# Performance work log

Measured on AMD Instinct MI355X. Metric: run time of the kernel, lower is better.

The kernel has to match this reference:

```python
import jax, jax.numpy as jnp
import numpy as np

B, T, D_IN, D_OUT = 4, 2048, 1024, 1024


def setup_inputs() -> dict:
    key = jax.random.key(0)
    k1, k2, k3, k4 = jax.random.split(key, 4)
    x = jax.random.normal(k1, (B, T, D_IN), dtype=jnp.float32)
    W_q = jax.random.normal(k2, (D_OUT, D_IN), dtype=jnp.float32) * 0.02
    W_k = jax.random.normal(k3, (D_OUT, D_IN), dtype=jnp.float32) * 0.02
    W_v = jax.random.normal(k4, (D_OUT, D_IN), dtype=jnp.float32) * 0.02
    return {"x": x, "W_q": W_q, "W_k": W_k, "W_v": W_v}


def reference(x, W_q, W_k, W_v):
    b, t, d_in = x.shape
    d_out = W_q.shape[0]
    # Linear projections (torch Linear: y = x @ W.T), no bias
    q = jnp.einsum("btd,od->bto", x, W_q)
    k = jnp.einsum("btd,od->bto", x, W_k)
    v = jnp.einsum("btd,od->bto", x, W_v)
    # Raw scores [b, t, t]
    scores = jnp.einsum("bqd,bkd->bqk", q, k)
    # Faithful to the source: tril with diagonal=1 => position i sees j <= i+1
    mask = jnp.tril(jnp.ones((t, t), dtype=bool), k=1)
    scores = jnp.where(mask, scores, -jnp.inf)
    # Scale by sqrt(d_out) (full d_out, single head), stable softmax
    attn = jax.nn.softmax(scores / jnp.sqrt(jnp.asarray(d_out, x.dtype)), axis=-1)
    # dropout=0.0 -> identity
    return jnp.einsum("bqk,bkd->bqd", attn, v)
```

## Files before the change

### kernel.cpp

```cpp
#include <hip/hip_runtime.h>
#include <hip/hip_bf16.h>

typedef unsigned short u16;
typedef __attribute__((ext_vector_type(8))) short short8v;
typedef __attribute__((ext_vector_type(4))) float float4v;

__device__ inline u16 f2b(float f) {
  __hip_bfloat16 h = __float2bfloat16(f);
  union { __hip_bfloat16 h; u16 s; } u;
  u.h = h;
  return u.s;
}

__device__ inline float b2f(u16 s) {
  union { u16 s[2]; float f; } u;
  u.s[0] = 0; u.s[1] = s;
  return u.f;
}

__device__ inline void gload_lds16(const u16* g, u16* l) {
  __builtin_amdgcn_global_load_lds(
      (const __attribute__((address_space(1))) void*)g,
      (__attribute__((address_space(3))) void*)l, 16, 0, 0);
}

__global__ __launch_bounds__(256) void cvt_f32_bf16(const float* __restrict__ in,
                                                    u16* __restrict__ out, int n4) {
  for (int i = blockIdx.x * blockDim.x + threadIdx.x; i < n4;
       i += gridDim.x * blockDim.x) {
    float4 v = ((const float4*)in)[i];
    ushort4 o;
    o.x = f2b(v.x); o.y = f2b(v.y); o.z = f2b(v.z); o.w = f2b(v.w);
    ((ushort4*)out)[i] = o;
  }
}

template <int MODE, typename CT>
__global__ __launch_bounds__(512)
void gemm4(const u16* __restrict__ A, int lda, long sA,
           const u16* __restrict__ B, int ldb, long sB,
           CT* __restrict__ C, int ldc, long sC, int K) {
  constexpr int BM = 256, BN = 128, BK = 64;
  constexpr int TILE_U16 = (BM + BN) * BK;
  constexpr int TILE_BYTES = TILE_U16 * 2;
  __shared__ __align__(16) u16 lds[3 * TILE_U16];

  const int z = blockIdx.z;
  A += (long)z * sA;
  B += (long)z * sB;

  int bx = blockIdx.x;
  if (MODE == 2) bx = gridDim.x - 1 - bx;
  const int m0 = bx * BM;
  const int n0 = blockIdx.y * BN;
  if (MODE == 1 && n0 > m0 + BM) return;
  int Keff = K;
  if (MODE == 2) Keff = min(m0 + BM + 1, K);
  const int nk = (Keff + BK - 1) >> 6;

  const int tid  = threadIdx.x;
  const int lane = tid & 63;
  const int wid  = tid >> 6;
  const int wr   = wid >> 1;
  const int wc   = wid & 1;

  const u16* gA[4]; int oA[4];
#pragma unroll
  for (int j = 0; j < 4; ++j) {
    int c = tid + j * 512;
    int r = c >> 3;
    int kg = ((c & 7) ^ (r & 7)) * 8;
    gA[j] = A + (long)(m0 + r) * lda + kg;
    oA[j] = c * 8;
  }
  const u16* gB[2]; int oB[2];
#pragma unroll
  for (int j = 0; j < 2; ++j) {
    int c = tid + j * 512;
    int r = c >> 3;
    int kg = ((c & 7) ^ (r & 7)) * 8;
    gB[j] = B + (long)(n0 + r) * ldb + kg;
    oB[j] = BM * BK + c * 8;
  }

  auto stageA3 = [&](int t, int buf) {
    const int k0 = t * BK;
    u16* base = lds + buf * TILE_U16;
    gload_lds16(gA[0] + k0, base + oA[0]);
    gload_lds16(gA[1] + k0, base + oA[1]);
    gload_lds16(gA[2] + k0, base + oA[2]);
  };
  auto stageRest = [&](int t, int buf) {
    const int k0 = t * BK;
    u16* base = lds + buf * TILE_U16;
    gload_lds16(gA[3] + k0, base + oA[3]);
    gload_lds16(gB[0] + k0, base + oB[0]);
    gload_lds16(gB[1] + k0, base + oB[1]);
  };

  const int rowA = wr * 64 + (lane & 15);
  const int rowB = wc * 64 + (lane & 15);
  const int msk  = (lane & 7) << 4;
  const int kl   = (lane >> 4) * 16;
  const int offA[2] = { rowA * 128 + ((kl) ^ msk),
                        rowA * 128 + ((64 + kl) ^ msk) };
  const int offB[2] = { 2 * BM * BK + rowB * 128 + ((kl) ^ msk),
                        2 * BM * BK + rowB * 128 + ((64 + kl) ^ msk) };

  float4v acc[4][4];
#pragma unroll
  for (int i = 0; i < 4; ++i)
#pragma unroll
    for (int j = 0; j < 4; ++j)
      acc[i][j] = (float4v){0.f, 0.f, 0.f, 0.f};

  stageA3(0, 0); stageRest(0, 0);
  if (nk > 1) { stageA3(1, 1); stageRest(1, 1); }

  int cur = 0;
  for (int t = 0; t < nk; ++t) {
    if (t + 1 < nk) asm volatile("s_waitcnt vmcnt(6)" ::: "memory");
    else            asm volatile("s_waitcnt vmcnt(0)" ::: "memory");
    __builtin_amdgcn_s_barrier();
    __builtin_amdgcn_sched_barrier(0);

    const char* bb = (const char*)lds + cur * TILE_BYTES;
    const int  nxt2 = (cur >= 1) ? cur - 1 : 2;
    const bool st   = (t + 2 < nk);

#pragma unroll
    for (int ks = 0; ks < 2; ++ks) {
      short8v a[4], b[4];
#pragma unroll
      for (int mi = 0; mi < 4; ++mi)
        a[mi] = *(const short8v*)(bb + offA[ks] + mi * 2048);
#pragma unroll
      for (int ni = 0; ni < 4; ++ni)
        b[ni] = *(const short8v*)(bb + offB[ks] + ni * 2048);
      if (ks == 0) { if (st) stageA3(t + 2, nxt2); }
      else         { if (st) stageRest(t + 2, nxt2); }
      __builtin_amdgcn_s_barrier();
      asm volatile("s_waitcnt lgkmcnt(0)" ::: "memory");
      __builtin_amdgcn_sched_barrier(0);
      __builtin_amdgcn_s_setprio(1);
#pragma unroll
      for (int mi = 0; mi < 4; ++mi)
#pragma unroll
        for (int ni = 0; ni < 4; ++ni)
          acc[mi][ni] = __builtin_amdgcn_mfma_f32_16x16x32_bf16(
              a[mi], b[ni], acc[mi][ni], 0, 0, 0);
      __builtin_amdgcn_s_setprio(0);
    }
    cur = (cur < 2) ? cur + 1 : 0;
  }

  CT* c = C + (long)z * sC;
  const int r0base = m0 + wr * 64 + ((lane >> 4) << 2);
  const int cbase  = n0 + wc * 64 + (lane & 15);
#pragma unroll
  for (int mi = 0; mi < 4; ++mi) {
#pragma unroll
    for (int ni = 0; ni < 4; ++ni) {
      const int r0 = r0base + mi * 16;
      const int cc = cbase + ni * 16;
#pragma unroll
      for (int r = 0; r < 4; ++r) {
        float v = acc[mi][ni][r];
        if constexpr (__is_same(CT, float)) c[(long)(r0 + r) * ldc + cc] = v;
        else                                c[(long)(r0 + r) * ldc + cc] = f2b(v);
      }
    }
  }
}

__global__ __launch_bounds__(256)
void softmax_kernel(u16* __restrict__ SP, int T) {
  const int  i    = blockIdx.x & (T - 1);
  const long base = (long)blockIdx.x * T;
  const int  nvis = min(i + 2, T);
  const int  capJ = min(T, ((i >> 8) << 8) + 320);
  const float scale = 0.03125f;

  __shared__ float red[4];

  const int j0 = threadIdx.x * 8;
  float v[8];
  float m = -INFINITY;
  if (j0 < nvis) {
    short8v raw = *(const short8v*)&SP[base + j0];
#pragma unroll
    for (int e = 0; e < 8; ++e) {
      float f = (j0 + e < nvis) ? b2f((u16)raw[e]) * scale : -INFINITY;
      v[e] = f;
      m = fmaxf(m, f);
    }
  }
#pragma unroll
  for (int o = 32; o; o >>= 1) m = fmaxf(m, __shfl_xor(m, o));
  const int wid = threadIdx.x >> 6;
  if ((threadIdx.x & 63) == 0) red[wid] = m;
  __syncthreads();
  m = fmaxf(fmaxf(red[0], red[1]), fmaxf(red[2], red[3]));
  __syncthreads();

  float s = 0.f;
  if (j0 < nvis) {
#pragma unroll
    for (int e = 0; e < 8; ++e) {
      float p = (j0 + e < nvis) ? __expf(v[e] - m) : 0.f;
      v[e] = p;
      s += p;
    }
  }
#pragma unroll
  for (int o = 32; o; o >>= 1) s += __shfl_xor(s, o);
  if ((threadIdx.x & 63) == 0) red[wid] = s;
  __syncthreads();
  s = red[0] + red[1] + red[2] + red[3];
  const float inv = 1.0f / s;

  if (j0 < capJ) {
    short8v o8;
#pragma unroll
    for (int e = 0; e < 8; ++e)
      o8[e] = (short)f2b((j0 + e < nvis) ? v[e] * inv : 0.f);
    *(short8v*)&SP[base + j0] = o8;
  }
}

extern "C" void kernel_launch(void* const* d_in, const int* in_sizes, int n_in,
                              void* d_out, int out_size, void* d_ws, size_t ws_size,
                              hipStream_t stream) {
  const float* x  = (const float*)d_in[0];
  const float* Wq = (const float*)d_in[1];
  const float* Wk = (const float*)d_in[2];
  const float* Wv = (const float*)d_in[3];
  float* out = (float*)d_out;

  const int B = 4, T = 2048, D = 1024;
  const int M = B * T;
  const long TT = (long)T * T;

  char* ws = (char*)d_ws;
  u16* qk  = (u16*)(ws);
  u16* vt  = (u16*)(ws + (32l << 20));
  u16* xb  = (u16*)(ws + (48l << 20));
  u16* wqk = (u16*)(ws + (64l << 20));
  u16* wv  = (u16*)(ws + (68l << 20));
  u16* S   = (u16*)(ws + (48l << 20));

  cvt_f32_bf16<<<2048, 256, 0, stream>>>(x,  xb,  (M * D) / 4);
  cvt_f32_bf16<<<512,  256, 0, stream>>>(Wq, wqk,               (D * D) / 4);
  cvt_f32_bf16<<<512,  256, 0, stream>>>(Wk, wqk + (long)D * D, (D * D) / 4);
  cvt_f32_bf16<<<512,  256, 0, stream>>>(Wv, wv,  (D * D) / 4);

  gemm4<0, u16><<<dim3(M / 256, 2 * D / 128, 1), 512, 0, stream>>>(
      xb, D, 0, wqk, D, 0, qk, 2 * D, 0, D);
  gemm4<0, u16><<<dim3(D / 256, M / 128, 1), 512, 0, stream>>>(
      wv, D, 0, xb, D, 0, vt, M, 0, D);

  gemm4<1, u16><<<dim3(T / 256, T / 128, B), 512, 0, stream>>>(
      qk, 2 * D, (long)T * 2 * D,
      qk + D, 2 * D, (long)T * 2 * D,
      S, T, TT, D);

  softmax_kernel<<<B * T, 256, 0, stream>>>(S, T);

  gemm4<2, float><<<dim3(T / 256, D / 128, B), 512, 0, stream>>>(
      S, T, TT,
      vt, M, T,
      out, D, (long)T * D, T);
}
```

Measured before the change: 175.9 us.

## Rework GEMM tiling to BN=256 with 2x4 warp grid and double buffering

```diff
diff --git a/kernel.cpp b/kernel.cpp
--- a/kernel.cpp
+++ b/kernel.cpp
@@ -35,15 +35,19 @@
   }
 }
 
-template <int MODE, typename CT>
+template <int WM, int MODE, typename CT>
 __global__ __launch_bounds__(512)
-void gemm4(const u16* __restrict__ A, int lda, long sA,
+void gemm5(const u16* __restrict__ A, int lda, long sA,
            const u16* __restrict__ B, int ldb, long sB,
            CT* __restrict__ C, int ldc, long sC, int K) {
-  constexpr int BM = 256, BN = 128, BK = 64;
-  constexpr int TILE_U16 = (BM + BN) * BK;
+  constexpr int BM = 2 * WM;
+  constexpr int BN = 256;
+  constexpr int A_U16 = BM * 64;
+  constexpr int TILE_U16 = (BM + BN) * 64;
   constexpr int TILE_BYTES = TILE_U16 * 2;
-  __shared__ __align__(16) u16 lds[3 * TILE_U16];
+  constexpr int LA = BM / 64;
+  constexpr int LB = 4;
+  __shared__ __align__(16) u16 lds[2 * TILE_U16];
 
   const int z = blockIdx.z;
   A += (long)z * sA;
@@ -56,89 +60,74 @@
   if (MODE == 1 && n0 > m0 + BM) return;
   int Keff = K;
   if (MODE == 2) Keff = min(m0 + BM + 1, K);
-  const int nk = (Keff + BK - 1) >> 6;
+  const int nk = (Keff + 63) >> 6;
 
   const int tid  = threadIdx.x;
   const int lane = tid & 63;
   const int wid  = tid >> 6;
-  const int wr   = wid >> 1;
-  const int wc   = wid & 1;
-
-  const u16* gA[4]; int oA[4];
-#pragma unroll
-  for (int j = 0; j < 4; ++j) {
+  const int wr   = wid >> 2;
+  const int wc   = wid & 3;
+
+  const u16* gsrc[LA + LB];
+  int loff[LA + LB];
+#pragma unroll
+  for (int j = 0; j < LA; ++j) {
     int c = tid + j * 512;
     int r = c >> 3;
     int kg = ((c & 7) ^ (r & 7)) * 8;
-    gA[j] = A + (long)(m0 + r) * lda + kg;
-    oA[j] = c * 8;
-  }
-  const u16* gB[2]; int oB[2];
-#pragma unroll
-  for (int j = 0; j < 2; ++j) {
+    gsrc[j] = A + (long)(m0 + r) * lda + kg;
+    loff[j] = c * 8;
+  }
+#pragma unroll
+  for (int j = 0; j < LB; ++j) {
     int c = tid + j * 512;
     int r = c >> 3;
     int kg = ((c & 7) ^ (r & 7)) * 8;
-    gB[j] = B + (long)(n0 + r) * ldb + kg;
-    oB[j] = BM * BK + c * 8;
-  }
-
-  auto stageA3 = [&](int t, int buf) {
-    const int k0 = t * BK;
-    u16* base = lds + buf * TILE_U16;
-    gload_lds16(gA[0] + k0, base + oA[0]);
-    gload_lds16(gA[1] + k0, base + oA[1]);
-    gload_lds16(gA[2] + k0, base + oA[2]);
-  };
-  auto stageRest = [&](int t, int buf) {
-    const int k0 = t * BK;
-    u16* base = lds + buf * TILE_U16;
-    gload_lds16(gA[3] + k0, base + oA[3]);
-    gload_lds16(gB[0] + k0, base + oB[0]);
-    gload_lds16(gB[1] + k0, base + oB[1]);
-  };
-
-  const int rowA = wr * 64 + (lane & 15);
-  const int rowB = wc * 64 + (lane & 15);
-  const int msk  = (lane & 7) << 4;
-  const int kl   = (lane >> 4) * 16;
-  const int offA[2] = { rowA * 128 + ((kl) ^ msk),
-                        rowA * 128 + ((64 + kl) ^ msk) };
-  const int offB[2] = { 2 * BM * BK + rowB * 128 + ((kl) ^ msk),
-                        2 * BM * BK + rowB * 128 + ((64 + kl) ^ msk) };
-
-  float4v acc[4][4];
-#pragma unroll
-  for (int i = 0; i < 4; ++i)
+    gsrc[LA + j] = B + (long)(n0 + r) * ldb + kg;
+    loff[LA + j] = A_U16 + c * 8;
+  }
+
+  const int kl  = (lane >> 4) * 16;
+  const int swz = (lane & 7) << 4;
+  const int kx0 = kl ^ swz;
+  const int kx1 = (64 + kl) ^ swz;
+  const int abase = (wr * WM + (lane & 15)) * 128;
+  const int bbase = BM * 128 + (wc * 64 + (lane & 15)) * 128;
+
+  float4v acc[WM / 16][4];
+#pragma unroll
+  for (int i = 0; i < WM / 16; ++i)
 #pragma unroll
     for (int j = 0; j < 4; ++j)
       acc[i][j] = (float4v){0.f, 0.f, 0.f, 0.f};
 
-  stageA3(0, 0); stageRest(0, 0);
-  if (nk > 1) { stageA3(1, 1); stageRest(1, 1); }
+#define STAGE_ALL(T_, DST_)                                                 \
+  {                                                                         \
+    _Pragma("unroll")                                                       \
+    for (int s = 0; s < LA + LB; ++s)                                       \
+      gload_lds16(gsrc[s] + (long)(T_) * 64, (DST_) + loff[s]);             \
+  }
+
+  STAGE_ALL(0, lds);
+  asm volatile("s_waitcnt vmcnt(0)" ::: "memory");
+  __builtin_amdgcn_s_barrier();
 
   int cur = 0;
   for (int t = 0; t < nk; ++t) {
-    if (t + 1 < nk) asm volatile("s_waitcnt vmcnt(6)" ::: "memory");
-    else            asm volatile("s_waitcnt vmcnt(0)" ::: "memory");
-    __builtin_amdgcn_s_barrier();
-    __builtin_amdgcn_sched_barrier(0);
-
     const char* bb = (const char*)lds + cur * TILE_BYTES;
-    const int  nxt2 = (cur >= 1) ? cur - 1 : 2;
-    const bool st   = (t + 2 < nk);
-
-#pragma unroll
-    for (int ks = 0; ks < 2; ++ks) {
-      short8v a[4], b[4];
+    u16* sb = lds + (cur ^ 1) * TILE_U16;
+    const bool st = (t + 1 < nk);
+    short8v b[4];
+
+    {
+      short8v a[4];
 #pragma unroll
       for (int mi = 0; mi < 4; ++mi)
-        a[mi] = *(const short8v*)(bb + offA[ks] + mi * 2048);
+        a[mi] = *(const short8v*)(bb + abase + mi * 2048 + kx0);
 #pragma unroll
       for (int ni = 0; ni < 4; ++ni)
-        b[ni] = *(const short8v*)(bb + offB[ks] + ni * 2048);
-      if (ks == 0) { if (st) stageA3(t + 2, nxt2); }
-      else         { if (st) stageRest(t + 2, nxt2); }
+        b[ni] = *(const short8v*)(bb + bbase + ni * 2048 + kx0);
+      if (st) STAGE_ALL(t + 1, sb);
       __builtin_amdgcn_s_barrier();
       asm volatile("s_waitcnt lgkmcnt(0)" ::: "memory");
       __builtin_amdgcn_sched_barrier(0);
@@ -150,15 +139,100 @@
           acc[mi][ni] = __builtin_amdgcn_mfma_f32_16x16x32_bf16(
               a[mi], b[ni], acc[mi][ni], 0, 0, 0);
       __builtin_amdgcn_s_setprio(0);
-    }
-    cur = (cur < 2) ? cur + 1 : 0;
-  }
+      __builtin_amdgcn_s_barrier();
+    }
+    if constexpr (WM == 128) {
+      {
+        short8v a[4];
+#pragma unroll
+        for (int mi = 0; mi < 4; ++mi)
+          a[mi] = *(const short8v*)(bb + abase + 8192 + mi * 2048 + kx0);
+        __builtin_amdgcn_s_barrier();
+        asm volatile("s_waitcnt lgkmcnt(0)" ::: "memory");
+        __builtin_amdgcn_sched_barrier(0);
+        __builtin_amdgcn_s_setprio(1);
+#pragma unroll
+        for (int mi = 0; mi < 4; ++mi)
+#pragma unroll
+          for (int ni = 0; ni < 4; ++ni)
+            acc[4 + mi][ni] = __builtin_amdgcn_mfma_f32_16x16x32_bf16(
+                a[mi], b[ni], acc[4 + mi][ni], 0, 0, 0);
+        __builtin_amdgcn_s_setprio(0);
+        __builtin_amdgcn_s_barrier();
+      }
+      {
+        short8v a[4];
+#pragma unroll
+        for (int mi = 0; mi < 4; ++mi)
+          a[mi] = *(const short8v*)(bb + abase + mi * 2048 + kx1);
+#pragma unroll
+        for (int ni = 0; ni < 4; ++ni)
+          b[ni] = *(const short8v*)(bb + bbase + ni * 2048 + kx1);
+        __builtin_amdgcn_s_barrier();
+        asm volatile("s_waitcnt lgkmcnt(0)" ::: "memory");
+        __builtin_amdgcn_sched_barrier(0);
+        __builtin_amdgcn_s_setprio(1);
+#pragma unroll
+        for (int mi = 0; mi < 4; ++mi)
+#pragma unroll
+          for (int ni = 0; ni < 4; ++ni)
+            acc[mi][ni] = __builtin_amdgcn_mfma_f32_16x16x32_bf16(
+                a[mi], b[ni], acc[mi][ni], 0, 0, 0);
+        __builtin_amdgcn_s_setprio(0);
+        __builtin_amdgcn_s_barrier();
+      }
+      {
+        short8v a[4];
+#pragma unroll
+        for (int mi = 0; mi < 4; ++mi)
+          a[mi] = *(const short8v*)(bb + abase + 8192 + mi * 2048 + kx1);
+        __builtin_amdgcn_s_barrier();
+        asm volatile("s_waitcnt lgkmcnt(0)" ::: "memory");
+        __builtin_amdgcn_sched_barrier(0);
+        __builtin_amdgcn_s_setprio(1);
+#pragma unroll
+        for (int mi = 0; mi < 4; ++mi)
+#pragma unroll
+          for (int ni = 0; ni < 4; ++ni)
+            acc[4 + mi][ni] = __builtin_amdgcn_mfma_f32_16x16x32_bf16(
+                a[mi], b[ni], acc[4 + mi][ni], 0, 0, 0);
+        __builtin_amdgcn_s_setprio(0);
+        asm volatile("s_waitcnt vmcnt(0)" ::: "memory");
+        __builtin_amdgcn_s_barrier();
+      }
+    } else {
+      {
+        short8v a[4];
+#pragma unroll
+        for (int mi = 0; mi < 4; ++mi)
+          a[mi] = *(const short8v*)(bb + abase + mi * 2048 + kx1);
+#pragma unroll
+        for (int ni = 0; ni < 4; ++ni)
+          b[ni] = *(const short8v*)(bb + bbase + ni * 2048 + kx1);
+        __builtin_amdgcn_s_barrier();
+        asm volatile("s_waitcnt lgkmcnt(0)" ::: "memory");
+        __builtin_amdgcn_sched_barrier(0);
+        __builtin_amdgcn_s_setprio(1);
+#pragma unroll
+        for (int mi = 0; mi < 4; ++mi)
+#pragma unroll
+          for (int ni = 0; ni < 4; ++ni)
+            acc[mi][ni] = __builtin_amdgcn_mfma_f32_16x16x32_bf16(
+                a[mi], b[ni], acc[mi][ni], 0, 0, 0);
+        __builtin_amdgcn_s_setprio(0);
+        asm volatile("s_waitcnt vmcnt(0)" ::: "memory");
+        __builtin_amdgcn_s_barrier();
+      }
+    }
+    cur ^= 1;
+  }
+#undef STAGE_ALL
 
   CT* c = C + (long)z * sC;
-  const int r0base = m0 + wr * 64 + ((lane >> 4) << 2);
+  const int r0base = m0 + wr * WM + ((lane >> 4) << 2);
   const int cbase  = n0 + wc * 64 + (lane & 15);
 #pragma unroll
-  for (int mi = 0; mi < 4; ++mi) {
+  for (int mi = 0; mi < WM / 16; ++mi) {
 #pragma unroll
     for (int ni = 0; ni < 4; ++ni) {
       const int r0 = r0base + mi * 16;
@@ -178,7 +252,7 @@
   const int  i    = blockIdx.x & (T - 1);
   const long base = (long)blockIdx.x * T;
   const int  nvis = min(i + 2, T);
-  const int  capJ = min(T, ((i >> 8) << 8) + 320);
+  const int  capJ = min(T, ((i >> 7) << 7) + 192);
   const float scale = 0.03125f;
 
   __shared__ float red[4];
@@ -254,19 +328,19 @@
   cvt_f32_bf16<<<512,  256, 0, stream>>>(Wk, wqk + (long)D * D, (D * D) / 4);
   cvt_f32_bf16<<<512,  256, 0, stream>>>(Wv, wv,  (D * D) / 4);
 
-  gemm4<0, u16><<<dim3(M / 256, 2 * D / 128, 1), 512, 0, stream>>>(
+  gemm5<128, 0, u16><<<dim3(M / 256, 2 * D / 256, 1), 512, 0, stream>>>(
       xb, D, 0, wqk, D, 0, qk, 2 * D, 0, D);
-  gemm4<0, u16><<<dim3(D / 256, M / 128, 1), 512, 0, stream>>>(
+  gemm5<64, 0, u16><<<dim3(D / 128, M / 256, 1), 512, 0, stream>>>(
       wv, D, 0, xb, D, 0, vt, M, 0, D);
 
-  gemm4<1, u16><<<dim3(T / 256, T / 128, B), 512, 0, stream>>>(
+  gemm5<64, 1, u16><<<dim3(T / 128, T / 256, B), 512, 0, stream>>>(
       qk, 2 * D, (long)T * 2 * D,
       qk + D, 2 * D, (long)T * 2 * D,
       S, T, TT, D);
 
   softmax_kernel<<<B * T, 256, 0, stream>>>(S, T);
 
-  gemm4<2, float><<<dim3(T / 256, D / 128, B), 512, 0, stream>>>(
+  gemm5<64, 2, float><<<dim3(T / 128, D / 256, B), 512, 0, stream>>>(
       S, T, TT,
       vt, M, T,
       out, D, (long)T * D, T);
```

New measurement: 172.6 us. Within noise of the previous version (-1.9%).

## Shrink GEMM tiles to 128x128 with 256 threads and double buffering

Applied to the files above, without the earlier changes.

```diff
diff --git a/kernel.cpp b/kernel.cpp
--- a/kernel.cpp
+++ b/kernel.cpp
@@ -36,14 +36,15 @@
 }
 
 template <int MODE, typename CT>
-__global__ __launch_bounds__(512)
-void gemm4(const u16* __restrict__ A, int lda, long sA,
+__global__ __launch_bounds__(256, 2)
+void gemm6(const u16* __restrict__ A, int lda, long sA,
            const u16* __restrict__ B, int ldb, long sB,
            CT* __restrict__ C, int ldc, long sC, int K) {
-  constexpr int BM = 256, BN = 128, BK = 64;
-  constexpr int TILE_U16 = (BM + BN) * BK;
+  constexpr int BM = 128, BN = 128;
+  constexpr int A_U16 = BM * 64;
+  constexpr int TILE_U16 = (BM + BN) * 64;
   constexpr int TILE_BYTES = TILE_U16 * 2;
-  __shared__ __align__(16) u16 lds[3 * TILE_U16];
+  __shared__ __align__(16) u16 lds[2 * TILE_U16];
 
   const int z = blockIdx.z;
   A += (long)z * sA;
@@ -56,7 +57,7 @@
   if (MODE == 1 && n0 > m0 + BM) return;
   int Keff = K;
   if (MODE == 2) Keff = min(m0 + BM + 1, K);
-  const int nk = (Keff + BK - 1) >> 6;
+  const int nk = (Keff + 63) >> 6;
 
   const int tid  = threadIdx.x;
   const int lane = tid & 63;
@@ -64,48 +65,38 @@
   const int wr   = wid >> 1;
   const int wc   = wid & 1;
 
-  const u16* gA[4]; int oA[4];
+  const u16* gsrc[8];
+  int loff[8];
 #pragma unroll
   for (int j = 0; j < 4; ++j) {
-    int c = tid + j * 512;
+    int c = tid + j * 256;
     int r = c >> 3;
     int kg = ((c & 7) ^ (r & 7)) * 8;
-    gA[j] = A + (long)(m0 + r) * lda + kg;
-    oA[j] = c * 8;
-  }
-  const u16* gB[2]; int oB[2];
-#pragma unroll
-  for (int j = 0; j < 2; ++j) {
-    int c = tid + j * 512;
+    gsrc[j] = A + (long)(m0 + r) * lda + kg;
+    loff[j] = c * 8;
+  }
+#pragma unroll
+  for (int j = 0; j < 4; ++j) {
+    int c = tid + j * 256;
     int r = c >> 3;
     int kg = ((c & 7) ^ (r & 7)) * 8;
-    gB[j] = B + (long)(n0 + r) * ldb + kg;
-    oB[j] = BM * BK + c * 8;
-  }
-
-  auto stageA3 = [&](int t, int buf) {
-    const int k0 = t * BK;
-    u16* base = lds + buf * TILE_U16;
-    gload_lds16(gA[0] + k0, base + oA[0]);
-    gload_lds16(gA[1] + k0, base + oA[1]);
-    gload_lds16(gA[2] + k0, base + oA[2]);
-  };
-  auto stageRest = [&](int t, int buf) {
-    const int k0 = t * BK;
-    u16* base = lds + buf * TILE_U16;
-    gload_lds16(gA[3] + k0, base + oA[3]);
-    gload_lds16(gB[0] + k0, base + oB[0]);
-    gload_lds16(gB[1] + k0, base + oB[1]);
-  };
-
-  const int rowA = wr * 64 + (lane & 15);
-  const int rowB = wc * 64 + (lane & 15);
-  const int msk  = (lane & 7) << 4;
-  const int kl   = (lane >> 4) * 16;
-  const int offA[2] = { rowA * 128 + ((kl) ^ msk),
-                        rowA * 128 + ((64 + kl) ^ msk) };
-  const int offB[2] = { 2 * BM * BK + rowB * 128 + ((kl) ^ msk),
-                        2 * BM * BK + rowB * 128 + ((64 + kl) ^ msk) };
+    gsrc[4 + j] = B + (long)(n0 + r) * ldb + kg;
+    loff[4 + j] = A_U16 + c * 8;
+  }
+
+#define STAGE_ALL(T_, DST_)                                                 \
+  {                                                                         \
+    _Pragma("unroll")                                                       \
+    for (int s = 0; s < 8; ++s)                                             \
+      gload_lds16(gsrc[s] + (long)(T_) * 64, (DST_) + loff[s]);             \
+  }
+
+  const int kl  = (lane >> 4) * 16;
+  const int swz = (lane & 7) << 4;
+  const int kx0 = kl ^ swz;
+  const int kx1 = (64 + kl) ^ swz;
+  const int abase = (wr * 64 + (lane & 15)) * 128;
+  const int bbase = 2 * A_U16 + (wc * 64 + (lane & 15)) * 128;
 
   float4v acc[4][4];
 #pragma unroll
@@ -114,45 +105,48 @@
     for (int j = 0; j < 4; ++j)
       acc[i][j] = (float4v){0.f, 0.f, 0.f, 0.f};
 
-  stageA3(0, 0); stageRest(0, 0);
-  if (nk > 1) { stageA3(1, 1); stageRest(1, 1); }
-
-  int cur = 0;
+  STAGE_ALL(0, lds);
+  asm volatile("s_waitcnt vmcnt(0)" ::: "memory");
+  __builtin_amdgcn_s_barrier();
+
   for (int t = 0; t < nk; ++t) {
-    if (t + 1 < nk) asm volatile("s_waitcnt vmcnt(6)" ::: "memory");
-    else            asm volatile("s_waitcnt vmcnt(0)" ::: "memory");
+    const char* bb = (const char*)lds + (t & 1) * TILE_BYTES;
+    u16* sb = lds + ((t & 1) ^ 1) * TILE_U16;
+
+    short8v a0[4], b0[4], a1[4], b1[4];
+#pragma unroll
+    for (int mi = 0; mi < 4; ++mi) {
+      a0[mi] = *(const short8v*)(bb + abase + mi * 2048 + kx0);
+      a1[mi] = *(const short8v*)(bb + abase + mi * 2048 + kx1);
+    }
+#pragma unroll
+    for (int ni = 0; ni < 4; ++ni) {
+      b0[ni] = *(const short8v*)(bb + bbase + ni * 2048 + kx0);
+      b1[ni] = *(const short8v*)(bb + bbase + ni * 2048 + kx1);
+    }
+    if (t + 1 < nk) STAGE_ALL(t + 1, sb);
+
+    asm volatile("s_waitcnt lgkmcnt(0)" ::: "memory");
+    __builtin_amdgcn_sched_barrier(0);
+    __builtin_amdgcn_s_setprio(1);
+#pragma unroll
+    for (int mi = 0; mi < 4; ++mi)
+#pragma unroll
+      for (int ni = 0; ni < 4; ++ni)
+        acc[mi][ni] = __builtin_amdgcn_mfma_f32_16x16x32_bf16(
+            a0[mi], b0[ni], acc[mi][ni], 0, 0, 0);
+#pragma unroll
+    for (int mi = 0; mi < 4; ++mi)
+#pragma unroll
+      for (int ni = 0; ni < 4; ++ni)
+        acc[mi][ni] = __builtin_amdgcn_mfma_f32_16x16x32_bf16(
+            a1[mi], b1[ni], acc[mi][ni], 0, 0, 0);
+    __builtin_amdgcn_s_setprio(0);
+
+    asm volatile("s_waitcnt vmcnt(0)" ::: "memory");
     __builtin_amdgcn_s_barrier();
-    __builtin_amdgcn_sched_barrier(0);
-
-    const char* bb = (const char*)lds + cur * TILE_BYTES;
-    const int  nxt2 = (cur >= 1) ? cur - 1 : 2;
-    const bool st   = (t + 2 < nk);
-
-#pragma unroll
-    for (int ks = 0; ks < 2; ++ks) {
-      short8v a[4], b[4];
-#pragma unroll
-      for (int mi = 0; mi < 4; ++mi)
-        a[mi] = *(const short8v*)(bb + offA[ks] + mi * 2048);
-#pragma unroll
-      for (int ni = 0; ni < 4; ++ni)
-        b[ni] = *(const short8v*)(bb + offB[ks] + ni * 2048);
-      if (ks == 0) { if (st) stageA3(t + 2, nxt2); }
-      else         { if (st) stageRest(t + 2, nxt2); }
-      __builtin_amdgcn_s_barrier();
-      asm volatile("s_waitcnt lgkmcnt(0)" ::: "memory");
-      __builtin_amdgcn_sched_barrier(0);
-      __builtin_amdgcn_s_setprio(1);
-#pragma unroll
-      for (int mi = 0; mi < 4; ++mi)
-#pragma unroll
-        for (int ni = 0; ni < 4; ++ni)
-          acc[mi][ni] = __builtin_amdgcn_mfma_f32_16x16x32_bf16(
-              a[mi], b[ni], acc[mi][ni], 0, 0, 0);
-      __builtin_amdgcn_s_setprio(0);
-    }
-    cur = (cur < 2) ? cur + 1 : 0;
-  }
+  }
+#undef STAGE_ALL
 
   CT* c = C + (long)z * sC;
   const int r0base = m0 + wr * 64 + ((lane >> 4) << 2);
@@ -178,7 +172,7 @@
   const int  i    = blockIdx.x & (T - 1);
   const long base = (long)blockIdx.x * T;
   const int  nvis = min(i + 2, T);
-  const int  capJ = min(T, ((i >> 8) << 8) + 320);
+  const int  capJ = min(T, ((i >> 7) << 7) + 192);
   const float scale = 0.03125f;
 
   __shared__ float red[4];
@@ -254,19 +248,19 @@
   cvt_f32_bf16<<<512,  256, 0, stream>>>(Wk, wqk + (long)D * D, (D * D) / 4);
   cvt_f32_bf16<<<512,  256, 0, stream>>>(Wv, wv,  (D * D) / 4);
 
-  gemm4<0, u16><<<dim3(M / 256, 2 * D / 128, 1), 512, 0, stream>>>(
+  gemm6<0, u16><<<dim3(M / 128, 2 * D / 128, 1), 256, 0, stream>>>(
       xb, D, 0, wqk, D, 0, qk, 2 * D, 0, D);
-  gemm4<0, u16><<<dim3(D / 256, M / 128, 1), 512, 0, stream>>>(
+  gemm6<0, u16><<<dim3(D / 128, M / 128, 1), 256, 0, stream>>>(
       wv, D, 0, xb, D, 0, vt, M, 0, D);
 
-  gemm4<1, u16><<<dim3(T / 256, T / 128, B), 512, 0, stream>>>(
+  gemm6<1, u16><<<dim3(T / 128, T / 128, B), 256, 0, stream>>>(
       qk, 2 * D, (long)T * 2 * D,
       qk + D, 2 * D, (long)T * 2 * D,
       S, T, TT, D);
 
   softmax_kernel<<<B * T, 256, 0, stream>>>(S, T);
 
-  gemm4<2, float><<<dim3(T / 256, D / 128, B), 512, 0, stream>>>(
+  gemm6<2, float><<<dim3(T / 128, D / 128, B), 256, 0, stream>>>(
       S, T, TT,
       vt, M, T,
       out, D, (long)T * D, T);
```

New measurement: 168.3 us. 4.3% less time.
